# Performance work log

Measured on AMD Instinct MI355X. Metric: run time of the kernel, lower is better.

The kernel has to match this reference:

```python
import jax, jax.numpy as jnp
import numpy as np

N_NODES = 100000


def setup_inputs() -> dict:
    key = jax.random.key(0)
    k1, k2, k3 = jax.random.split(key, 3)
    x = jax.random.normal(k1, (N_NODES, 64), dtype=jnp.float32)
    edge_index = jax.random.randint(k2, (2, 1250000), 0, N_NODES, dtype=jnp.int64)
    W = jax.random.normal(k3, (128, 64), dtype=jnp.float32) * (1.0 / np.sqrt(128.0))
    b = jnp.zeros((64,), dtype=jnp.float32)
    return {"x": x, "edge_index": edge_index, "W": W, "b": b}


def reference(x, edge_index, W, b):
    n = x.shape[0]
    row, col = edge_index[0], edge_index[1]
    # scatter-add neighbor features onto destination nodes
    neigh = jax.ops.segment_sum(x[row], col, num_segments=n)          # [n, d]
    count = jax.ops.segment_sum(jnp.ones_like(col, dtype=x.dtype), col, num_segments=n)
    count = jnp.where(count == 0, jnp.asarray(1.0, x.dtype), count)   # avoid div-by-zero
    neigh = neigh / count[:, None]                                    # mean aggregation
    x_aggr = jnp.concatenate([x, neigh], axis=-1)                     # [n, 2d]
    out = x_aggr @ W + b                                              # [n, out_dim]
    return jax.nn.relu(out)  # dropout=0.0 (eval) -> identity
```

## Files before the change

### kernel.cpp

```cpp
#include <hip/hip_runtime.h>

#define D 64
#define NPB 64
#define THREADS 512
#define CAP 64

typedef int v4i __attribute__((ext_vector_type(4)));

__device__ __forceinline__ unsigned short f2bf(float f) {
  unsigned u = __float_as_uint(f);
  return (unsigned short)((u + 0x7FFFu + ((u >> 16) & 1u)) >> 16);
}
__device__ __forceinline__ float bf2f(unsigned short h) {
  return __uint_as_float(((unsigned)h) << 16);
}

__global__ __launch_bounds__(256) void prep0_kernel(
    const float* __restrict__ x, ushort* __restrict__ xh,
    int* __restrict__ cnt, int n, int total4) {
  int t = blockIdx.x * blockDim.x + threadIdx.x;
  int nth = gridDim.x * blockDim.x;
  for (int i = t; i < n; i += nth) cnt[i] = 0;
  for (int i = t; i < total4; i += nth) {
    float4 v = ((const float4*)x)[i];
    ushort4 h;
    h.x = f2bf(v.x); h.y = f2bf(v.y); h.z = f2bf(v.z); h.w = f2bf(v.w);
    ((ushort4*)xh)[i] = h;
  }
}

__global__ __launch_bounds__(256) void fill_xcd_kernel(
    const int* __restrict__ ei, int* __restrict__ cnt,
    int* __restrict__ bucket, int e, int qpc) {
  const int myx = blockIdx.x & 7;
  const int chunk = blockIdx.x >> 3;
  const int quads = e >> 2;
  const v4i* row4 = (const v4i*)ei;
  const v4i* col4 = (const v4i*)(ei + e);
  int qend = chunk * qpc + qpc;
  if (qend > quads) qend = quads;
  for (int q = chunk * qpc + threadIdx.x; q < qend; q += 256) {
    v4i r = __builtin_nontemporal_load(&row4[q]);
    v4i c = __builtin_nontemporal_load(&col4[q]);
    if (((c.x >> 11) & 7) == myx) {
      int p = atomicAdd(&cnt[c.x], 1);
      if (p < CAP) bucket[(size_t)c.x * CAP + p] = r.x * D;
    }
    if (((c.y >> 11) & 7) == myx) {
      int p = atomicAdd(&cnt[c.y], 1);
      if (p < CAP) bucket[(size_t)c.y * CAP + p] = r.y * D;
    }
    if (((c.z >> 11) & 7) == myx) {
      int p = atomicAdd(&cnt[c.z], 1);
      if (p < CAP) bucket[(size_t)c.z * CAP + p] = r.z * D;
    }
    if (((c.w >> 11) & 7) == myx) {
      int p = atomicAdd(&cnt[c.w], 1);
      if (p < CAP) bucket[(size_t)c.w * CAP + p] = r.w * D;
    }
  }
}

__global__ __launch_bounds__(THREADS, 8) void fused_bf_kernel(
    const float* __restrict__ x, const ushort* __restrict__ xh,
    const int* __restrict__ cnt, const float* __restrict__ W,
    const float* __restrict__ b, float* __restrict__ out, int n) {
  __shared__ __align__(16) float xs[NPB * 128];

  const int lane = threadIdx.x & 63;
  const int wid  = threadIdx.x >> 6;
  const int base = blockIdx.x * NPB;
  const int* bucket = (const int*)out;
  const ushort* xpl = xh + lane;

  for (int m = 0; m < 8; ++m) {
    int nl = wid * 8 + m;
    int node = base + nl;
    if (node < n) {
      int dg = cnt[node];
      int dc = dg < CAP ? dg : CAP;
      int bk = bucket[(size_t)node * CAP + lane];
      float xown = x[(size_t)node * D + lane];
      float s0 = 0.f, s1 = 0.f, s2 = 0.f, s3 = 0.f;
      float s4 = 0.f, s5 = 0.f, s6 = 0.f, s7 = 0.f;
      int p = 0;
      for (; p + 8 <= dc; p += 8) {
        int a0 = __shfl(bk, p),     a1 = __shfl(bk, p + 1);
        int a2 = __shfl(bk, p + 2), a3 = __shfl(bk, p + 3);
        int a4 = __shfl(bk, p + 4), a5 = __shfl(bk, p + 5);
        int a6 = __shfl(bk, p + 6), a7 = __shfl(bk, p + 7);
        s0 += bf2f(xpl[a0]); s1 += bf2f(xpl[a1]);
        s2 += bf2f(xpl[a2]); s3 += bf2f(xpl[a3]);
        s4 += bf2f(xpl[a4]); s5 += bf2f(xpl[a5]);
        s6 += bf2f(xpl[a6]); s7 += bf2f(xpl[a7]);
      }
      for (; p + 4 <= dc; p += 4) {
        int a0 = __shfl(bk, p),     a1 = __shfl(bk, p + 1);
        int a2 = __shfl(bk, p + 2), a3 = __shfl(bk, p + 3);
        s0 += bf2f(xpl[a0]); s1 += bf2f(xpl[a1]);
        s2 += bf2f(xpl[a2]); s3 += bf2f(xpl[a3]);
      }
      for (; p < dc; ++p)
        s0 += bf2f(xpl[__shfl(bk, p)]);
      float sum = ((s0 + s1) + (s2 + s3)) + ((s4 + s5) + (s6 + s7));
      float inv = (dg > 0) ? (1.0f / (float)dg) : 0.0f;
      xs[nl * 128 + lane]      = xown;
      xs[nl * 128 + 64 + lane] = sum * inv;
    } else {
      xs[nl * 128 + lane]      = 0.0f;
      xs[nl * 128 + 64 + lane] = 0.0f;
    }
  }
  __syncthreads();

  const int col = lane;
  float bias = b[col];
  float acc[8];
#pragma unroll
  for (int m = 0; m < 8; ++m) acc[m] = bias;

  for (int k = 0; k < 128; k += 4) {
    float w0 = W[(k + 0) * 64 + col];
    float w1 = W[(k + 1) * 64 + col];
    float w2 = W[(k + 2) * 64 + col];
    float w3 = W[(k + 3) * 64 + col];
#pragma unroll
    for (int m = 0; m < 8; ++m) {
      int nl = wid + m * 8;
      float4 xv = *(const float4*)&xs[nl * 128 + k];
      acc[m] = fmaf(xv.x, w0, acc[m]);
      acc[m] = fmaf(xv.y, w1, acc[m]);
      acc[m] = fmaf(xv.z, w2, acc[m]);
      acc[m] = fmaf(xv.w, w3, acc[m]);
    }
  }

#pragma unroll
  for (int m = 0; m < 8; ++m) {
    int node = base + wid + m * 8;
    if (node < n)
      out[(size_t)node * D + col] = fmaxf(acc[m], 0.0f);
  }
}

__global__ __launch_bounds__(256) void fill_cap_kernel(
    const int* __restrict__ ei, int* __restrict__ cnt,
    int* __restrict__ bucket, int e) {
  int t = blockIdx.x * blockDim.x + threadIdx.x;
  if (t * 4 >= e) return;
  int4 r4 = ((const int4*)ei)[t];
  int4 c4 = ((const int4*)(ei + e))[t];
  int p0 = atomicAdd(&cnt[c4.x], 1);
  int p1 = atomicAdd(&cnt[c4.y], 1);
  int p2 = atomicAdd(&cnt[c4.z], 1);
  int p3 = atomicAdd(&cnt[c4.w], 1);
  if (p0 < CAP) bucket[(size_t)c4.x * CAP + p0] = r4.x;
  if (p1 < CAP) bucket[(size_t)c4.y * CAP + p1] = r4.y;
  if (p2 < CAP) bucket[(size_t)c4.z * CAP + p2] = r4.z;
  if (p3 < CAP) bucket[(size_t)c4.w * CAP + p3] = r4.w;
}

__global__ __launch_bounds__(THREADS, 8) void fused_cap_kernel(
    const float* __restrict__ x, const int* __restrict__ cnt,
    const float* __restrict__ W, const float* __restrict__ b,
    float* __restrict__ out, int n) {
  __shared__ __align__(16) float xs[NPB * 128];
  const int lane = threadIdx.x & 63;
  const int wid  = threadIdx.x >> 6;
  const int base = blockIdx.x * NPB;
  const int* bucket = (const int*)out;

  for (int m = 0; m < 8; ++m) {
    int nl = wid * 8 + m;
    int node = base + nl;
    if (node < n) {
      int dg = cnt[node];
      int dc = dg < CAP ? dg : CAP;
      int bk = bucket[(size_t)node * CAP + lane];
      float xown = x[(size_t)node * D + lane];
      float s0 = 0.f, s1 = 0.f, s2 = 0.f, s3 = 0.f;
      int p = 0;
      for (; p + 4 <= dc; p += 4) {
        int a0 = __shfl(bk, p),     a1 = __shfl(bk, p + 1);
        int a2 = __shfl(bk, p + 2), a3 = __shfl(bk, p + 3);
        s0 += x[(size_t)a0 * D + lane];
        s1 += x[(size_t)a1 * D + lane];
        s2 += x[(size_t)a2 * D + lane];
        s3 += x[(size_t)a3 * D + lane];
      }
      for (; p < dc; ++p)
        s0 += x[(size_t)__shfl(bk, p) * D + lane];
      float sum = (s0 + s1) + (s2 + s3);
      float inv = (dg > 0) ? (1.0f / (float)dg) : 0.0f;
      xs[nl * 128 + lane]      = xown;
      xs[nl * 128 + 64 + lane] = sum * inv;
    } else {
      xs[nl * 128 + lane]      = 0.0f;
      xs[nl * 128 + 64 + lane] = 0.0f;
    }
  }
  __syncthreads();

  const int col = lane;
  float bias = b[col];
  float acc[8];
#pragma unroll
  for (int m = 0; m < 8; ++m) acc[m] = bias;
  for (int k = 0; k < 128; k += 4) {
    float w0 = W[(k + 0) * 64 + col];
    float w1 = W[(k + 1) * 64 + col];
    float w2 = W[(k + 2) * 64 + col];
    float w3 = W[(k + 3) * 64 + col];
#pragma unroll
    for (int m = 0; m < 8; ++m) {
      int nl = wid + m * 8;
      float4 xv = *(const float4*)&xs[nl * 128 + k];
      acc[m] = fmaf(xv.x, w0, acc[m]);
      acc[m] = fmaf(xv.y, w1, acc[m]);
      acc[m] = fmaf(xv.z, w2, acc[m]);
      acc[m] = fmaf(xv.w, w3, acc[m]);
    }
  }
#pragma unroll
  for (int m = 0; m < 8; ++m) {
    int node = base + wid + m * 8;
    if (node < n)
      out[(size_t)node * D + col] = fmaxf(acc[m], 0.0f);
  }
}

extern "C" void kernel_launch(void* const* d_in, const int* in_sizes, int n_in,
                              void* d_out, int out_size, void* d_ws, size_t ws_size,
                              hipStream_t stream) {
  const float* x = (const float*)d_in[0];
  const int* ei = (const int*)d_in[1];
  const float* W = (const float*)d_in[2];
  const float* b = (const float*)d_in[3];
  float* out = (float*)d_out;

  int n = in_sizes[0] / D;
  int e = in_sizes[1] / 2;
  int nblocks = (n + NPB - 1) / NPB;

  size_t xh_bytes = (size_t)n * D * sizeof(ushort);
  size_t need = xh_bytes + (size_t)n * sizeof(int) + 256;

  if (ws_size >= need && (e & 3) == 0 && n <= (1 << 17)) {
    ushort* xh = (ushort*)d_ws;
    int* cnt = (int*)((char*)d_ws + ((xh_bytes + 255) & ~(size_t)255));

    int total4 = n * D / 4;
    prep0_kernel<<<2048, 256, 0, stream>>>(x, xh, cnt, n, total4);

    int quads = e >> 2;
    int qpc = (quads + 255) / 256;
    fill_xcd_kernel<<<256 * 8, 256, 0, stream>>>(ei, cnt, (int*)d_out, e, qpc);

    fused_bf_kernel<<<nblocks, THREADS, 0, stream>>>(x, xh, cnt, W, b, out, n);
  } else {
    int* cnt = (int*)d_ws;
    (void)hipMemsetAsync(cnt, 0, (size_t)n * sizeof(int), stream);
    int quads = e / 4;
    fill_cap_kernel<<<(quads + 255) / 256, 256, 0, stream>>>(ei, cnt, (int*)d_out, e);
    fused_cap_kernel<<<nblocks, THREADS, 0, stream>>>(x, cnt, W, b, out, n);
  }
}
```

Baseline: 212.1 us.

## Replace scalar FMA linear layer with split-bf16 MFMA using swizzled LDS

The dense projection after aggregation now runs on MFMA 16x16x32 bf16 instructions instead of per-lane FP32 FMAs. To keep near-FP32 accuracy, activations and weights are split into hi/lo bf16 parts, and three MFMA products (hi*hi, lo*hi, hi*lo) are accumulated. W is pre-transposed and split in the prep kernel into workspace buffers. The LDS tile is stored as swizzled bf16 to avoid bank conflicts. This cuts the ALU cost of the GEMM phase but adds split conversions and a small amount of extra prep work. The kernel is likely dominated by the gather, so the overall benefit may be limited.

```diff
diff --git a/kernel.cpp b/kernel.cpp
--- a/kernel.cpp
+++ b/kernel.cpp
@@ -6,6 +6,8 @@
 #define CAP 64
 
 typedef int v4i __attribute__((ext_vector_type(4)));
+typedef short bf16x8 __attribute__((ext_vector_type(8)));
+typedef float f32x4 __attribute__((ext_vector_type(4)));
 
 __device__ __forceinline__ unsigned short f2bf(float f) {
   unsigned u = __float_as_uint(f);
@@ -14,13 +16,29 @@
 __device__ __forceinline__ float bf2f(unsigned short h) {
   return __uint_as_float(((unsigned)h) << 16);
 }
+__device__ __forceinline__ void bfsplit(float v, unsigned short& hi, unsigned short& lo) {
+  unsigned u = __float_as_uint(v);
+  hi = (unsigned short)(u >> 16);
+  float r = v - __uint_as_float(u & 0xFFFF0000u);
+  lo = f2bf(r);
+}
 
 __global__ __launch_bounds__(256) void prep0_kernel(
     const float* __restrict__ x, ushort* __restrict__ xh,
-    int* __restrict__ cnt, int n, int total4) {
+    int* __restrict__ cnt, const float* __restrict__ W,
+    ushort* __restrict__ wth, ushort* __restrict__ wtl,
+    int n, int total4) {
   int t = blockIdx.x * blockDim.x + threadIdx.x;
   int nth = gridDim.x * blockDim.x;
   for (int i = t; i < n; i += nth) cnt[i] = 0;
+  for (int i = t; i < 2 * D * D; i += nth) {
+    int nn = i >> 7, k = i & 127;
+    float v = W[k * D + nn];
+    unsigned short hi, lo;
+    bfsplit(v, hi, lo);
+    wth[i] = hi;
+    wtl[i] = lo;
+  }
   for (int i = t; i < total4; i += nth) {
     float4 v = ((const float4*)x)[i];
     ushort4 h;
@@ -63,9 +81,11 @@
 
 __global__ __launch_bounds__(THREADS, 8) void fused_bf_kernel(
     const float* __restrict__ x, const ushort* __restrict__ xh,
-    const int* __restrict__ cnt, const float* __restrict__ W,
+    const int* __restrict__ cnt,
+    const ushort* __restrict__ wth, const ushort* __restrict__ wtl,
     const float* __restrict__ b, float* __restrict__ out, int n) {
-  __shared__ __align__(16) float xs[NPB * 128];
+  __shared__ __align__(16) ushort xsh[NPB * 128];
+  __shared__ __align__(16) ushort xsl[NPB * 128];
 
   const int lane = threadIdx.x & 63;
   const int wid  = threadIdx.x >> 6;
@@ -76,6 +96,8 @@
   for (int m = 0; m < 8; ++m) {
     int nl = wid * 8 + m;
     int node = base + nl;
+    int koff = nl * 128;
+    int k0 = lane ^ ((nl & 7) << 3);
     if (node < n) {
       int dg = cnt[node];
       int dc = dg < CAP ? dg : CAP;
@@ -104,42 +126,64 @@
         s0 += bf2f(xpl[__shfl(bk, p)]);
       float sum = ((s0 + s1) + (s2 + s3)) + ((s4 + s5) + (s6 + s7));
       float inv = (dg > 0) ? (1.0f / (float)dg) : 0.0f;
-      xs[nl * 128 + lane]      = xown;
-      xs[nl * 128 + 64 + lane] = sum * inv;
+      float mean = sum * inv;
+      unsigned short h, l;
+      bfsplit(xown, h, l);
+      xsh[koff + k0] = h;       xsl[koff + k0] = l;
+      bfsplit(mean, h, l);
+      xsh[koff + 64 + k0] = h;  xsl[koff + 64 + k0] = l;
     } else {
-      xs[nl * 128 + lane]      = 0.0f;
-      xs[nl * 128 + 64 + lane] = 0.0f;
+      xsh[koff + k0] = 0;       xsl[koff + k0] = 0;
+      xsh[koff + 64 + k0] = 0;  xsl[koff + 64 + k0] = 0;
     }
   }
   __syncthreads();
 
-  const int col = lane;
-  float bias = b[col];
-  float acc[8];
+  const int mt   = wid >> 1;
+  const int nb   = (wid & 1) * 32;
+  const int lrow = lane & 15;
+  const int kgrp = (lane >> 4) * 8;
+
+  const int arow = mt * 16 + lrow;
+  const int aswz = (arow & 7) << 3;
+  const int abase = arow * 128;
+
+  const ushort* wh0 = wth + (nb + lrow) * 128;
+  const ushort* wh1 = wth + (nb + 16 + lrow) * 128;
+  const ushort* wl0 = wtl + (nb + lrow) * 128;
+  const ushort* wl1 = wtl + (nb + 16 + lrow) * 128;
+
+  float bias0 = b[nb + lrow];
+  float bias1 = b[nb + 16 + lrow];
+  f32x4 acc0 = {bias0, bias0, bias0, bias0};
+  f32x4 acc1 = {bias1, bias1, bias1, bias1};
+
+#pragma unroll 2
+  for (int ks = 0; ks < 4; ++ks) {
+    int kb = ks * 32 + kgrp;
+    int ke = abase + (kb ^ aswz);
+    bf16x8 ah = *(const bf16x8*)&xsh[ke];
+    bf16x8 al = *(const bf16x8*)&xsl[ke];
+    bf16x8 w0h = *(const bf16x8*)(wh0 + kb);
+    bf16x8 w1h = *(const bf16x8*)(wh1 + kb);
+    acc0 = __builtin_amdgcn_mfma_f32_16x16x32_bf16(ah, w0h, acc0, 0, 0, 0);
+    acc1 = __builtin_amdgcn_mfma_f32_16x16x32_bf16(ah, w1h, acc1, 0, 0, 0);
+    acc0 = __builtin_amdgcn_mfma_f32_16x16x32_bf16(al, w0h, acc0, 0, 0, 0);
+    acc1 = __builtin_amdgcn_mfma_f32_16x16x32_bf16(al, w1h, acc1, 0, 0, 0);
+    bf16x8 w0l = *(const bf16x8*)(wl0 + kb);
+    bf16x8 w1l = *(const bf16x8*)(wl1 + kb);
+    acc0 = __builtin_amdgcn_mfma_f32_16x16x32_bf16(ah, w0l, acc0, 0, 0, 0);
+    acc1 = __builtin_amdgcn_mfma_f32_16x16x32_bf16(ah, w1l, acc1, 0, 0, 0);
+  }
+
+  const int drow = (lane >> 4) * 4;
 #pragma unroll
-  for (int m = 0; m < 8; ++m) acc[m] = bias;
-
-  for (int k = 0; k < 128; k += 4) {
-    float w0 = W[(k + 0) * 64 + col];
-    float w1 = W[(k + 1) * 64 + col];
-    float w2 = W[(k + 2) * 64 + col];
-    float w3 = W[(k + 3) * 64 + col];
-#pragma unroll
-    for (int m = 0; m < 8; ++m) {
-      int nl = wid + m * 8;
-      float4 xv = *(const float4*)&xs[nl * 128 + k];
-      acc[m] = fmaf(xv.x, w0, acc[m]);
-      acc[m] = fmaf(xv.y, w1, acc[m]);
-      acc[m] = fmaf(xv.z, w2, acc[m]);
-      acc[m] = fmaf(xv.w, w3, acc[m]);
-    }
-  }
-
-#pragma unroll
-  for (int m = 0; m < 8; ++m) {
-    int node = base + wid + m * 8;
-    if (node < n)
-      out[(size_t)node * D + col] = fmaxf(acc[m], 0.0f);
+  for (int r = 0; r < 4; ++r) {
+    int node = base + mt * 16 + drow + r;
+    if (node < n) {
+      out[(size_t)node * D + nb + lrow]      = fmaxf(acc0[r], 0.0f);
+      out[(size_t)node * D + nb + 16 + lrow] = fmaxf(acc1[r], 0.0f);
+    }
   }
 }
 
@@ -243,20 +287,27 @@
   int nblocks = (n + NPB - 1) / NPB;
 
   size_t xh_bytes = (size_t)n * D * sizeof(ushort);
-  size_t need = xh_bytes + (size_t)n * sizeof(int) + 256;
+  size_t off = (xh_bytes + 255) & ~(size_t)255;
+  size_t cnt_off = off;
+  off += (((size_t)n * sizeof(int)) + 255) & ~(size_t)255;
+  size_t wth_off = off;  off += 2 * D * D * sizeof(ushort);
+  size_t wtl_off = off;  off += 2 * D * D * sizeof(ushort);
+  size_t need = off + 256;
 
   if (ws_size >= need && (e & 3) == 0 && n <= (1 << 17)) {
-    ushort* xh = (ushort*)d_ws;
-    int* cnt = (int*)((char*)d_ws + ((xh_bytes + 255) & ~(size_t)255));
+    ushort* xh  = (ushort*)d_ws;
+    int* cnt    = (int*)((char*)d_ws + cnt_off);
+    ushort* wth = (ushort*)((char*)d_ws + wth_off);
+    ushort* wtl = (ushort*)((char*)d_ws + wtl_off);
 
     int total4 = n * D / 4;
-    prep0_kernel<<<2048, 256, 0, stream>>>(x, xh, cnt, n, total4);
+    prep0_kernel<<<2048, 256, 0, stream>>>(x, xh, cnt, W, wth, wtl, n, total4);
 
     int quads = e >> 2;
     int qpc = (quads + 255) / 256;
     fill_xcd_kernel<<<256 * 8, 256, 0, stream>>>(ei, cnt, (int*)d_out, e, qpc);
 
-    fused_bf_kernel<<<nblocks, THREADS, 0, stream>>>(x, xh, cnt, W, b, out, n);
+    fused_bf_kernel<<<nblocks, THREADS, 0, stream>>>(x, xh, cnt, wth, wtl, b, out, n);
   } else {
     int* cnt = (int*)d_ws;
     (void)hipMemsetAsync(cnt, 0, (size_t)n * sizeof(int), stream);
```

Result: faster. 205.8 us (-3.0%).
